# Kernel tuning notes

Measured on AMD Instinct MI355X. Metric: run time of the kernel, lower is better.

The kernel has to match this reference:

```python
import jax, jax.numpy as jnp
import numpy as np

N = 100000
E = 1600000
IN_DIM = 256
HID = 128
LAYERS = 8
ALPHA = 0.1
THETA = 0.5


def setup_inputs() -> dict:
    key = jax.random.key(0)
    ks = jax.random.split(key, 6)
    x = jax.random.normal(ks[0], (N, IN_DIM), dtype=jnp.float32)
    edge_index = jax.random.randint(ks[1], (2, E), 0, N, dtype=jnp.int64)
    W_in = jax.random.normal(ks[2], (IN_DIM, HID), dtype=jnp.float32) / np.sqrt(IN_DIM)
    b_in = jnp.zeros((HID,), dtype=jnp.float32)
    convs_W = jax.random.normal(ks[3], (LAYERS, HID, HID), dtype=jnp.float32) / np.sqrt(HID)
    W_out = jax.random.normal(ks[4], (HID, 1), dtype=jnp.float32) / np.sqrt(HID)
    b_out = jnp.zeros((1,), dtype=jnp.float32)
    return {"x": x, "edge_index": edge_index, "W_in": W_in, "b_in": b_in,
            "convs_W": convs_W, "W_out": W_out, "b_out": b_out}


def reference(x, edge_index, W_in, b_in, convs_W, W_out, b_out):
    row = edge_index[0]  # source nodes
    col = edge_index[1]  # destination nodes
    # gcn_norm with self-loops: deg = in-degree + 1
    deg = jax.ops.segment_sum(jnp.ones((E,), dtype=jnp.float32), col, num_segments=N) + 1.0
    dinv = jax.lax.rsqrt(deg)
    norm = dinv[row] * dinv[col]            # [E] edge weights
    self_norm = dinv * dinv                 # [N] self-loop weights (1/deg)

    def propagate(h):
        # Ahat @ h : gather-scale-scatter over edges + self-loop term
        msgs = h[row] * norm[:, None]       # [E, HID]
        return jax.ops.segment_sum(msgs, col, num_segments=N) + h * self_norm[:, None]

    h0 = jax.nn.relu(x @ W_in + b_in)       # initial residual
    h = h0
    for i in range(LAYERS):
        agg = propagate(h)
        s = (1.0 - ALPHA) * agg + ALPHA * h0
        beta = float(np.log(THETA / (i + 1) + 1.0))
        h = jax.nn.relu((1.0 - beta) * s + beta * (s @ convs_W[i]))
    return (h @ W_out + b_out).squeeze(-1)  # [N]
```

## Files before the change

### kernel.cpp

```cpp
#include <hip/hip_runtime.h>
#include <math.h>

#define HID 128
#define NB 32
#define SBST 136
#define CSH 9
#define MCH 8192
#define GOFF (32 * SBST)
#define CAP 1024

typedef unsigned int uint32;
typedef unsigned short ushort_t;
typedef __attribute__((ext_vector_type(8))) short bf16x8;
typedef __attribute__((ext_vector_type(4))) float f32x4;

__device__ __forceinline__ unsigned short f2bf(float f) {
    unsigned u = __float_as_uint(f);
    u += 0x7FFF + ((u >> 16) & 1);
    return (unsigned short)(u >> 16);
}
__device__ __forceinline__ float bf_lo(uint32 u) { return __uint_as_float(u << 16); }
__device__ __forceinline__ float bf_hi(uint32 u) { return __uint_as_float(u & 0xFFFF0000u); }

__global__ void degree_k(const int* __restrict__ col, int* __restrict__ counts, int E) {
    int e = blockIdx.x * 256 + threadIdx.x;
    if (e < E) atomicAdd(&counts[col[e]], 1);
}

__global__ void scan1_k(const int* __restrict__ counts, int* __restrict__ row_ptr,
                        int* __restrict__ blocksums, float* __restrict__ dinv, int N) {
    __shared__ int tmp[256];
    int t = threadIdx.x;
    int i = blockIdx.x * 256 + t;
    int v = (i < N) ? counts[i] : 0;
    if (i < N) dinv[i] = rsqrtf((float)v + 1.0f);
    tmp[t] = v;
    __syncthreads();
    for (int off = 1; off < 256; off <<= 1) {
        int x = (t >= off) ? tmp[t - off] : 0;
        __syncthreads();
        tmp[t] += x;
        __syncthreads();
    }
    if (i < N) row_ptr[i] = tmp[t] - v;
    if (t == 255) blocksums[blockIdx.x] = tmp[t];
}

__global__ void scan2_k(const int* __restrict__ blocksums, int* __restrict__ blockoffs, int nb) {
    __shared__ int tmp[512];
    int t = threadIdx.x;
    int v = (t < nb) ? blocksums[t] : 0;
    tmp[t] = v;
    __syncthreads();
    for (int off = 1; off < 512; off <<= 1) {
        int x = (t >= off) ? tmp[t - off] : 0;
        __syncthreads();
        tmp[t] += x;
        __syncthreads();
    }
    if (t < nb) blockoffs[t] = tmp[t] - v;
}

__global__ void scan3_k(int* __restrict__ row_ptr, int* __restrict__ cursor,
                        int* __restrict__ ccursor,
                        const int* __restrict__ blockoffs, int N, int E) {
    int i = blockIdx.x * 256 + threadIdx.x;
    if (i < N) {
        int v = row_ptr[i] + blockoffs[blockIdx.x];
        row_ptr[i] = v;
        cursor[i] = v;
        if ((i & ((1 << CSH) - 1)) == 0) ccursor[i >> CSH] = v;
    }
    if (i == 0) row_ptr[N] = E;
}

__global__ __launch_bounds__(256) void multisplit_k(const int* __restrict__ row,
                                                    const int* __restrict__ col,
                                                    int* __restrict__ ccursor,
                                                    int2* __restrict__ ebuf,
                                                    int E, int NCO) {
    __shared__ int lcnt[256];
    __shared__ int gbase[256];
    __shared__ int lpos[256];
    int t = threadIdx.x;
    int e0 = blockIdx.x * MCH;
    lcnt[t] = 0;
    lpos[t] = 0;
    __syncthreads();
    for (int i = t; i < MCH; i += 256) {
        int e = e0 + i;
        if (e < E) atomicAdd(&lcnt[col[e] >> CSH], 1);
    }
    __syncthreads();
    if (t < NCO && lcnt[t] > 0) gbase[t] = atomicAdd(&ccursor[t], lcnt[t]);
    __syncthreads();
    for (int i = t; i < MCH; i += 256) {
        int e = e0 + i;
        if (e < E) {
            int c = col[e];
            int b = c >> CSH;
            int p = atomicAdd(&lpos[b], 1);
            ebuf[gbase[b] + p] = make_int2(row[e], c);
        }
    }
}

__global__ void cfinal_k(const int2* __restrict__ ebuf, const int* __restrict__ row_ptr,
                         int* __restrict__ cursor, int* __restrict__ srcS, int N) {
    int b = blockIdx.x;
    int n0 = b << CSH;
    int n1 = n0 + (1 << CSH);
    if (n1 > N) n1 = N;
    int beg = row_ptr[n0];
    int end = row_ptr[n1];
    for (int i = beg + threadIdx.x; i < end; i += 256) {
        int2 p = ebuf[i];
        int pos = atomicAdd(&cursor[p.y], 1);
        srcS[pos] = p.x;
    }
}

__global__ void wprep_k(const float* __restrict__ convs, short* __restrict__ Wt) {
    int idx = blockIdx.x * 256 + threadIdx.x;
    if (idx >= 8 * 128 * 128) return;
    int l = idx >> 14;
    int r = idx & 16383;
    int k = r >> 7;
    int n = r & 127;
    float beta = logf(0.5f / (float)(l + 1) + 1.0f);
    float v = beta * convs[idx] + ((k == n) ? (1.0f - beta) : 0.0f);
    Wt[(l << 14) + (n << 7) + k] = (short)f2bf(v);
}

__global__ void winprep_k(const float* __restrict__ Win, short* __restrict__ Winb) {
    int idx = blockIdx.x * 256 + threadIdx.x;
    if (idx >= 256 * 128) return;
    int k = idx >> 7;
    int n = idx & 127;
    Winb[n * 256 + k] = (short)f2bf(Win[idx]);
}

__global__ __launch_bounds__(256) void h0_k(const float* __restrict__ x,
                                            const short* __restrict__ Winb,
                                            const float* __restrict__ bin,
                                            const float* __restrict__ dinv,
                                            ushort_t* __restrict__ h0b,
                                            ushort_t* __restrict__ g,
                                            int N) {
    __shared__ float xsf[NB * 256];
    __shared__ float s_dv[NB];
    int t = threadIdx.x;
    int lane = t & 63, wv = t >> 6;
    int base = blockIdx.x * NB;

    if (t < NB) s_dv[t] = (base + t < N) ? dinv[base + t] : 1.f;

    if (base + NB <= N) {
        const float* xblk = x + (size_t)base * 256;
#pragma unroll
        for (int it = 0; it < 8; it++) {
            int m = wv * 8 + it;
            const float* src = xblk + (size_t)m * 256 + ((lane ^ (m & 7)) << 2);
            __builtin_amdgcn_global_load_lds(
                (const __attribute__((address_space(1))) unsigned int*)src,
                (__attribute__((address_space(3))) unsigned int*)&xsf[m * 256],
                16, 0, 0);
        }
    } else {
        for (int idx = t; idx < NB * 64; idx += 256) {
            int m = idx >> 6;
            int c16 = idx & 63;
            int nn = base + m;
            float4 v = make_float4(0.f, 0.f, 0.f, 0.f);
            if (nn < N) v = *(const float4*)&x[(size_t)nn * 256 + c16 * 4];
            *(float4*)&xsf[m * 256 + ((c16 ^ (m & 7)) << 2)] = v;
        }
    }
    __syncthreads();

    int mt = (wv & 1) * 16;
    int jb = wv >> 1;
    int lrow = lane & 15;
    int lq = lane >> 4;
    int r = mt + lrow;
    f32x4 acc0 = {0.f, 0.f, 0.f, 0.f};
    f32x4 acc1 = {0.f, 0.f, 0.f, 0.f};
    f32x4 acc2 = {0.f, 0.f, 0.f, 0.f};
    f32x4 acc3 = {0.f, 0.f, 0.f, 0.f};
#pragma unroll
    for (int ks = 0; ks < 8; ks++) {
        int c16a = ks * 8 + lq * 2;
        f32x4 va = *(const f32x4*)&xsf[r * 256 + (((c16a + 0) ^ (r & 7)) << 2)];
        f32x4 vb = *(const f32x4*)&xsf[r * 256 + (((c16a + 1) ^ (r & 7)) << 2)];
        bf16x8 a;
        a[0] = (short)f2bf(va[0]); a[1] = (short)f2bf(va[1]);
        a[2] = (short)f2bf(va[2]); a[3] = (short)f2bf(va[3]);
        a[4] = (short)f2bf(vb[0]); a[5] = (short)f2bf(vb[1]);
        a[6] = (short)f2bf(vb[2]); a[7] = (short)f2bf(vb[3]);
        bf16x8 b0 = *(const bf16x8*)&Winb[((jb + 0) * 16 + lrow) * 256 + ks * 32 + lq * 8];
        bf16x8 b1 = *(const bf16x8*)&Winb[((jb + 2) * 16 + lrow) * 256 + ks * 32 + lq * 8];
        bf16x8 b2 = *(const bf16x8*)&Winb[((jb + 4) * 16 + lrow) * 256 + ks * 32 + lq * 8];
        bf16x8 b3 = *(const bf16x8*)&Winb[((jb + 6) * 16 + lrow) * 256 + ks * 32 + lq * 8];
        acc0 = __builtin_amdgcn_mfma_f32_16x16x32_bf16(a, b0, acc0, 0, 0, 0);
        acc1 = __builtin_amdgcn_mfma_f32_16x16x32_bf16(a, b1, acc1, 0, 0, 0);
        acc2 = __builtin_amdgcn_mfma_f32_16x16x32_bf16(a, b2, acc2, 0, 0, 0);
        acc3 = __builtin_amdgcn_mfma_f32_16x16x32_bf16(a, b3, acc3, 0, 0, 0);
    }

    __syncthreads();
    short* sb = (short*)xsf;
#pragma unroll
    for (int q = 0; q < 4; q++) {
        f32x4 accq = (q == 0) ? acc0 : (q == 1) ? acc1 : (q == 2) ? acc2 : acc3;
        int j0 = (jb + 2 * q) * 16;
        float bj = bin[j0 + lrow];
#pragma unroll
        for (int rr = 0; rr < 4; rr++) {
            int rowm = mt + lq * 4 + rr;
            float h = fmaxf(accq[rr] + bj, 0.f);
            sb[rowm * SBST + j0 + lrow] = (short)f2bf(h);
            sb[GOFF + rowm * SBST + j0 + lrow] = (short)f2bf(s_dv[rowm] * h);
        }
    }
    __syncthreads();
    for (int idx = t; idx < NB * 16; idx += 256) {
        int rowm = idx >> 4;
        int c = (idx & 15) * 8;
        int dst = base + rowm;
        if (dst < N) {
            *(bf16x8*)&h0b[(size_t)dst * HID + c] = *(const bf16x8*)&sb[rowm * SBST + c];
            *(bf16x8*)&g[(size_t)dst * HID + c]   = *(const bf16x8*)&sb[GOFF + rowm * SBST + c];
        }
    }
}

__global__ __launch_bounds__(256, 6) void layer_k(const ushort_t* __restrict__ g_in,
                                                  ushort_t* __restrict__ g_out,
                                                  const ushort_t* __restrict__ h0b,
                                                  const float* __restrict__ dinv,
                                                  const int* __restrict__ row_ptr,
                                                  const int* __restrict__ srcS,
                                                  const short* __restrict__ Wtb,
                                                  int N) {
    __shared__ int   s_idx[CAP + 16];
    __shared__ int   s_rp[NB + 1];
    __shared__ short s_bf[NB * SBST];
    __shared__ float s_dv[NB];
    int t = threadIdx.x;
    int lane = t & 63;
    int wv = t >> 6;
    int base = blockIdx.x * NB;

    if (t < NB + 1) s_rp[t] = row_ptr[min(base + t, N)];
    if (t < NB) s_dv[t] = (base + t < N) ? dinv[base + t] : 1.f;
    int blk_beg = row_ptr[base];
    int blk_end = row_ptr[min(base + NB, N)];
    int nE = blk_end - blk_beg;
    int nL = nE < CAP ? nE : CAP;
    for (int i = t; i < nL; i += 256) s_idx[i] = srcS[blk_beg + i];
    if (t < 16) s_idx[nL + t] = 0;
    __syncthreads();

    const char* gbp = (const char*)g_in;
    uint32 lb = (uint32)(lane << 2);
    for (int m = wv; m < NB; m += 4) {
        int dst = base + m;
        if (dst >= N) {
            *(uint32*)&s_bf[m * SBST + lane * 2] = 0;
            continue;
        }
        float dv = s_dv[m];
        uint32 gd = ((const uint32*)(g_in + (size_t)dst * HID))[lane];
        uint32 hu = ((const uint32*)(h0b + (size_t)dst * HID))[lane];
        float ax = bf_lo(gd), ay = bf_hi(gd);
        int beg = s_rp[m], end = s_rp[m + 1];
        int lend = end - blk_beg;
        if (lend <= CAP) {
            for (int e = beg - blk_beg; e < lend; e += 16) {
                int rem = lend - e;
                int i0  = s_idx[e + 0];
                int i1  = s_idx[e + 1];
                int i2  = s_idx[e + 2];
                int i3  = s_idx[e + 3];
                int i4  = s_idx[e + 4];
                int i5  = s_idx[e + 5];
                int i6  = s_idx[e + 6];
                int i7  = s_idx[e + 7];
                int i8  = s_idx[e + 8];
                int i9  = s_idx[e + 9];
                int i10 = s_idx[e + 10];
                int i11 = s_idx[e + 11];
                int i12 = s_idx[e + 12];
                int i13 = s_idx[e + 13];
                int i14 = s_idx[e + 14];
                int i15 = s_idx[e + 15];
                uint32 g0  = *(const uint32*)(gbp + (((uint32)i0  << 8) | lb));
                uint32 g1  = *(const uint32*)(gbp + (((uint32)i1  << 8) | lb));
                uint32 g2  = *(const uint32*)(gbp + (((uint32)i2  << 8) | lb));
                uint32 g3  = *(const uint32*)(gbp + (((uint32)i3  << 8) | lb));
                uint32 g4  = *(const uint32*)(gbp + (((uint32)i4  << 8) | lb));
                uint32 g5  = *(const uint32*)(gbp + (((uint32)i5  << 8) | lb));
                uint32 g6  = *(const uint32*)(gbp + (((uint32)i6  << 8) | lb));
                uint32 g7  = *(const uint32*)(gbp + (((uint32)i7  << 8) | lb));
                uint32 g8  = *(const uint32*)(gbp + (((uint32)i8  << 8) | lb));
                uint32 g9  = *(const uint32*)(gbp + (((uint32)i9  << 8) | lb));
                uint32 g10 = *(const uint32*)(gbp + (((uint32)i10 << 8) | lb));
                uint32 g11 = *(const uint32*)(gbp + (((uint32)i11 << 8) | lb));
                uint32 g12 = *(const uint32*)(gbp + (((uint32)i12 << 8) | lb));
                uint32 g13 = *(const uint32*)(gbp + (((uint32)i13 << 8) | lb));
                uint32 g14 = *(const uint32*)(gbp + (((uint32)i14 << 8) | lb));
                uint32 g15 = *(const uint32*)(gbp + (((uint32)i15 << 8) | lb));
                ax += bf_lo(g0); ay += bf_hi(g0);
                if (rem > 1)  { ax += bf_lo(g1);  ay += bf_hi(g1);  }
                if (rem > 2)  { ax += bf_lo(g2);  ay += bf_hi(g2);  }
                if (rem > 3)  { ax += bf_lo(g3);  ay += bf_hi(g3);  }
                if (rem > 4)  { ax += bf_lo(g4);  ay += bf_hi(g4);  }
                if (rem > 5)  { ax += bf_lo(g5);  ay += bf_hi(g5);  }
                if (rem > 6)  { ax += bf_lo(g6);  ay += bf_hi(g6);  }
                if (rem > 7)  { ax += bf_lo(g7);  ay += bf_hi(g7);  }
                if (rem > 8)  { ax += bf_lo(g8);  ay += bf_hi(g8);  }
                if (rem > 9)  { ax += bf_lo(g9);  ay += bf_hi(g9);  }
                if (rem > 10) { ax += bf_lo(g10); ay += bf_hi(g10); }
                if (rem > 11) { ax += bf_lo(g11); ay += bf_hi(g11); }
                if (rem > 12) { ax += bf_lo(g12); ay += bf_hi(g12); }
                if (rem > 13) { ax += bf_lo(g13); ay += bf_hi(g13); }
                if (rem > 14) { ax += bf_lo(g14); ay += bf_hi(g14); }
                if (rem > 15) { ax += bf_lo(g15); ay += bf_hi(g15); }
            }
        } else {
            for (int e = beg; e < end; e += 16) {
                int rem = end - e;
                int last = end - 1;
#pragma unroll
                for (int k = 0; k < 16; k++) {
                    if (k < rem) {
                        int ii = e + k;
                        int sn = srcS[ii > last ? last : ii];
                        uint32 gg = *(const uint32*)(gbp + (((uint32)sn << 8) | lb));
                        ax += bf_lo(gg); ay += bf_hi(gg);
                    }
                }
            }
        }
        float sc = 0.9f * dv;
        float sx = sc * ax + 0.1f * bf_lo(hu);
        float sy = sc * ay + 0.1f * bf_hi(hu);
        uint32 pk = ((uint32)f2bf(sy) << 16) | (uint32)f2bf(sx);
        *(uint32*)&s_bf[m * SBST + lane * 2] = pk;
    }
    __syncthreads();

    int mt = (wv & 1) * 16;
    int jb = wv >> 1;
    int lrow = lane & 15;
    int lq = lane >> 4;
    f32x4 acc0 = {0.f, 0.f, 0.f, 0.f};
    f32x4 acc1 = {0.f, 0.f, 0.f, 0.f};
    f32x4 acc2 = {0.f, 0.f, 0.f, 0.f};
    f32x4 acc3 = {0.f, 0.f, 0.f, 0.f};
#pragma unroll
    for (int ks = 0; ks < 4; ks++) {
        bf16x8 a = *(const bf16x8*)&s_bf[(mt + lrow) * SBST + ks * 32 + lq * 8];
        bf16x8 b0 = *(const bf16x8*)&Wtb[((jb + 0) * 16 + lrow) * 128 + ks * 32 + lq * 8];
        bf16x8 b1 = *(const bf16x8*)&Wtb[((jb + 2) * 16 + lrow) * 128 + ks * 32 + lq * 8];
        bf16x8 b2 = *(const bf16x8*)&Wtb[((jb + 4) * 16 + lrow) * 128 + ks * 32 + lq * 8];
        bf16x8 b3 = *(const bf16x8*)&Wtb[((jb + 6) * 16 + lrow) * 128 + ks * 32 + lq * 8];
        acc0 = __builtin_amdgcn_mfma_f32_16x16x32_bf16(a, b0, acc0, 0, 0, 0);
        acc1 = __builtin_amdgcn_mfma_f32_16x16x32_bf16(a, b1, acc1, 0, 0, 0);
        acc2 = __builtin_amdgcn_mfma_f32_16x16x32_bf16(a, b2, acc2, 0, 0, 0);
        acc3 = __builtin_amdgcn_mfma_f32_16x16x32_bf16(a, b3, acc3, 0, 0, 0);
    }

    __syncthreads();
#pragma unroll
    for (int q = 0; q < 4; q++) {
        f32x4 accq = (q == 0) ? acc0 : (q == 1) ? acc1 : (q == 2) ? acc2 : acc3;
        int j0 = (jb + 2 * q) * 16;
#pragma unroll
        for (int r = 0; r < 4; r++) {
            int rowm = mt + lq * 4 + r;
            float h = fmaxf(accq[r], 0.f);
            s_bf[rowm * SBST + j0 + lrow] = (short)f2bf(s_dv[rowm] * h);
        }
    }
    __syncthreads();
    for (int idx = t; idx < NB * 16; idx += 256) {
        int rowm = idx >> 4;
        int c = (idx & 15) * 8;
        int dst = base + rowm;
        if (dst < N)
            *(bf16x8*)&g_out[(size_t)dst * HID + c] = *(const bf16x8*)&s_bf[rowm * SBST + c];
    }
}

__global__ void out_k(const ushort_t* __restrict__ g, const float* __restrict__ dinv,
                      const float* __restrict__ Wout, const float* __restrict__ bout,
                      float* __restrict__ out, int N) {
    int t = threadIdx.x;
    int lane = t & 63;
    int wv = t >> 6;
    int n = blockIdx.x * 4 + wv;
    if (n >= N) return;
    uint32 u = ((const uint32*)(g + (size_t)n * HID))[lane];
    float v = bf_lo(u) * Wout[lane * 2] + bf_hi(u) * Wout[lane * 2 + 1];
#pragma unroll
    for (int off = 32; off > 0; off >>= 1) v += __shfl_down(v, off, 64);
    if (lane == 0) out[n] = v / dinv[n] + bout[0];
}

extern "C" void kernel_launch(void* const* d_in, const int* in_sizes, int n_in,
                              void* d_out, int out_size, void* d_ws, size_t ws_size,
                              hipStream_t stream) {
    const float* x    = (const float*)d_in[0];
    const int*   ei   = (const int*)d_in[1];
    const float* Win  = (const float*)d_in[2];
    const float* bin  = (const float*)d_in[3];
    const float* convs= (const float*)d_in[4];
    const float* Wout = (const float*)d_in[5];
    const float* bout = (const float*)d_in[6];

    int N = in_sizes[0] / 256;
    int E = in_sizes[1] / 2;
    const int* row = ei;
    const int* col = ei + E;

    char* ws = (char*)d_ws;
    size_t off = 0;
    auto alloc = [&](size_t bytes) -> char* {
        char* p = ws + off;
        off = (off + bytes + 255) & ~(size_t)255;
        return p;
    };
    int NCO = (N + (1 << CSH) - 1) >> CSH;
    int*      counts    = (int*)alloc((size_t)N * 4);
    int*      row_ptr   = (int*)alloc((size_t)(N + 1) * 4);
    int*      cursor    = (int*)alloc((size_t)N * 4);
    int*      ccursor   = (int*)alloc((size_t)NCO * 4);
    int*      blocksums = (int*)alloc(512 * 4);
    int*      blockoffs = (int*)alloc(512 * 4);
    float*    dinv      = (float*)alloc((size_t)N * 4);
    int*      srcS      = (int*)alloc((size_t)E * 4);
    short*    Wt        = (short*)alloc((size_t)8 * 128 * 128 * 2);
    short*    Winb      = (short*)alloc((size_t)256 * 128 * 2);
    ushort_t* h0b       = (ushort_t*)alloc((size_t)N * HID * 2);
    ushort_t* gA        = (ushort_t*)alloc((size_t)N * HID * 2);
    ushort_t* gB        = (ushort_t*)alloc((size_t)N * HID * 2);
    int2*     ebuf      = (int2*)gB;

    int eb = (E + 255) / 256;
    int nb = (N + 255) / 256;
    int mb = (E + MCH - 1) / MCH;

    hipMemsetAsync(counts, 0, (size_t)N * 4, stream);
    degree_k<<<eb, 256, 0, stream>>>(col, counts, E);
    scan1_k<<<nb, 256, 0, stream>>>(counts, row_ptr, blocksums, dinv, N);
    scan2_k<<<1, 512, 0, stream>>>(blocksums, blockoffs, nb);
    scan3_k<<<nb, 256, 0, stream>>>(row_ptr, cursor, ccursor, blockoffs, N, E);
    multisplit_k<<<mb, 256, 0, stream>>>(row, col, ccursor, ebuf, E, NCO);
    cfinal_k<<<NCO, 256, 0, stream>>>(ebuf, row_ptr, cursor, srcS, N);
    wprep_k<<<512, 256, 0, stream>>>(convs, Wt);
    winprep_k<<<128, 256, 0, stream>>>(Win, Winb);

    int gb = (N + NB - 1) / NB;
    h0_k<<<gb, 256, 0, stream>>>(x, Winb, bin, dinv, h0b, gA, N);

    ushort_t* gin = gA;
    ushort_t* gout = gB;
    for (int i = 0; i < 8; i++) {
        layer_k<<<gb, 256, 0, stream>>>(gin, gout, h0b, dinv, row_ptr, srcS,
                                        Wt + (size_t)i * 128 * 128, N);
        ushort_t* tp = gin; gin = gout; gout = tp;
    }
    out_k<<<(N + 3) / 4, 256, 0, stream>>>(gin, dinv, Wout, bout, (float*)d_out, N);
}
```

Before: 1.006 ms.

## Gather two edges per wave with 8-byte lanes and half-wave reduction

The aggregation loop now splits each wave into two halves. Each half gathers a different edge's 256-byte row using 8-byte loads per lane, and the halves are combined with a cross-half shuffle. Partial tail groups are padded by repeating the last neighbor, and the surplus copies are subtracted afterward, so the per-edge branches go away. Launch bounds are lowered to 4 waves per SIMD to allow more registers for the wider gathers, which may reduce occupancy. The correction also adds rounding differences from subtracting repeated bf16 values.

```diff
diff --git a/kernel.cpp b/kernel.cpp
--- a/kernel.cpp
+++ b/kernel.cpp
@@ -234,7 +234,7 @@
     }
 }
 
-__global__ __launch_bounds__(256, 6) void layer_k(const ushort_t* __restrict__ g_in,
+__global__ __launch_bounds__(256, 4) void layer_k(const ushort_t* __restrict__ g_in,
                                                   ushort_t* __restrict__ g_out,
                                                   const ushort_t* __restrict__ h0b,
                                                   const float* __restrict__ dinv,
@@ -242,7 +242,7 @@
                                                   const int* __restrict__ srcS,
                                                   const short* __restrict__ Wtb,
                                                   int N) {
-    __shared__ int   s_idx[CAP + 16];
+    __shared__ int   s_idx[CAP];
     __shared__ int   s_rp[NB + 1];
     __shared__ short s_bf[NB * SBST];
     __shared__ float s_dv[NB];
@@ -258,95 +258,126 @@
     int nE = blk_end - blk_beg;
     int nL = nE < CAP ? nE : CAP;
     for (int i = t; i < nL; i += 256) s_idx[i] = srcS[blk_beg + i];
-    if (t < 16) s_idx[nL + t] = 0;
     __syncthreads();
 
     const char* gbp = (const char*)g_in;
-    uint32 lb = (uint32)(lane << 2);
+    const char* hbp = (const char*)h0b;
+    int c = lane & 31;
+    int half = lane >> 5;
+    uint32 cb = (uint32)(c << 3);
+
     for (int m = wv; m < NB; m += 4) {
         int dst = base + m;
         if (dst >= N) {
-            *(uint32*)&s_bf[m * SBST + lane * 2] = 0;
+            if (lane < 32) *(uint2*)&s_bf[m * SBST + c * 4] = make_uint2(0u, 0u);
             continue;
         }
         float dv = s_dv[m];
-        uint32 gd = ((const uint32*)(g_in + (size_t)dst * HID))[lane];
-        uint32 hu = ((const uint32*)(h0b + (size_t)dst * HID))[lane];
-        float ax = bf_lo(gd), ay = bf_hi(gd);
+        uint2 sg = make_uint2(0u, 0u), sh = make_uint2(0u, 0u);
+        if (lane < 32) {
+            sg = *(const uint2*)(gbp + (((size_t)dst) << 8) + cb);
+            sh = *(const uint2*)(hbp + (((size_t)dst) << 8) + cb);
+        }
         int beg = s_rp[m], end = s_rp[m + 1];
-        int lend = end - blk_beg;
-        if (lend <= CAP) {
-            for (int e = beg - blk_beg; e < lend; e += 16) {
-                int rem = lend - e;
-                int i0  = s_idx[e + 0];
-                int i1  = s_idx[e + 1];
-                int i2  = s_idx[e + 2];
-                int i3  = s_idx[e + 3];
-                int i4  = s_idx[e + 4];
-                int i5  = s_idx[e + 5];
-                int i6  = s_idx[e + 6];
-                int i7  = s_idx[e + 7];
-                int i8  = s_idx[e + 8];
-                int i9  = s_idx[e + 9];
-                int i10 = s_idx[e + 10];
-                int i11 = s_idx[e + 11];
-                int i12 = s_idx[e + 12];
-                int i13 = s_idx[e + 13];
-                int i14 = s_idx[e + 14];
-                int i15 = s_idx[e + 15];
-                uint32 g0  = *(const uint32*)(gbp + (((uint32)i0  << 8) | lb));
-                uint32 g1  = *(const uint32*)(gbp + (((uint32)i1  << 8) | lb));
-                uint32 g2  = *(const uint32*)(gbp + (((uint32)i2  << 8) | lb));
-                uint32 g3  = *(const uint32*)(gbp + (((uint32)i3  << 8) | lb));
-                uint32 g4  = *(const uint32*)(gbp + (((uint32)i4  << 8) | lb));
-                uint32 g5  = *(const uint32*)(gbp + (((uint32)i5  << 8) | lb));
-                uint32 g6  = *(const uint32*)(gbp + (((uint32)i6  << 8) | lb));
-                uint32 g7  = *(const uint32*)(gbp + (((uint32)i7  << 8) | lb));
-                uint32 g8  = *(const uint32*)(gbp + (((uint32)i8  << 8) | lb));
-                uint32 g9  = *(const uint32*)(gbp + (((uint32)i9  << 8) | lb));
-                uint32 g10 = *(const uint32*)(gbp + (((uint32)i10 << 8) | lb));
-                uint32 g11 = *(const uint32*)(gbp + (((uint32)i11 << 8) | lb));
-                uint32 g12 = *(const uint32*)(gbp + (((uint32)i12 << 8) | lb));
-                uint32 g13 = *(const uint32*)(gbp + (((uint32)i13 << 8) | lb));
-                uint32 g14 = *(const uint32*)(gbp + (((uint32)i14 << 8) | lb));
-                uint32 g15 = *(const uint32*)(gbp + (((uint32)i15 << 8) | lb));
-                ax += bf_lo(g0); ay += bf_hi(g0);
-                if (rem > 1)  { ax += bf_lo(g1);  ay += bf_hi(g1);  }
-                if (rem > 2)  { ax += bf_lo(g2);  ay += bf_hi(g2);  }
-                if (rem > 3)  { ax += bf_lo(g3);  ay += bf_hi(g3);  }
-                if (rem > 4)  { ax += bf_lo(g4);  ay += bf_hi(g4);  }
-                if (rem > 5)  { ax += bf_lo(g5);  ay += bf_hi(g5);  }
-                if (rem > 6)  { ax += bf_lo(g6);  ay += bf_hi(g6);  }
-                if (rem > 7)  { ax += bf_lo(g7);  ay += bf_hi(g7);  }
-                if (rem > 8)  { ax += bf_lo(g8);  ay += bf_hi(g8);  }
-                if (rem > 9)  { ax += bf_lo(g9);  ay += bf_hi(g9);  }
-                if (rem > 10) { ax += bf_lo(g10); ay += bf_hi(g10); }
-                if (rem > 11) { ax += bf_lo(g11); ay += bf_hi(g11); }
-                if (rem > 12) { ax += bf_lo(g12); ay += bf_hi(g12); }
-                if (rem > 13) { ax += bf_lo(g13); ay += bf_hi(g13); }
-                if (rem > 14) { ax += bf_lo(g14); ay += bf_hi(g14); }
-                if (rem > 15) { ax += bf_lo(g15); ay += bf_hi(g15); }
-            }
-        } else {
-            for (int e = beg; e < end; e += 16) {
-                int rem = end - e;
-                int last = end - 1;
-#pragma unroll
-                for (int k = 0; k < 16; k++) {
-                    if (k < rem) {
-                        int ii = e + k;
-                        int sn = srcS[ii > last ? last : ii];
-                        uint32 gg = *(const uint32*)(gbp + (((uint32)sn << 8) | lb));
-                        ax += bf_lo(gg); ay += bf_hi(gg);
+        int deg = end - beg;
+        float a0 = 0.f, a1 = 0.f, a2 = 0.f, a3 = 0.f;
+        bool fastp = (end - blk_beg) <= nL;
+        if (deg > 0) {
+            int nfull = deg >> 4;
+            if (fastp) {
+                int e = beg - blk_beg;
+                int lastI = e + deg - 1;
+                for (int r = 0; r < nfull; ++r, e += 16) {
+                    int ixx[8];
+#pragma unroll
+                    for (int p = 0; p < 8; p++) ixx[p] = s_idx[e + 2 * p + half];
+                    uint2 gvv[8];
+#pragma unroll
+                    for (int p = 0; p < 8; p++)
+                        gvv[p] = *(const uint2*)(gbp + (((size_t)(uint32)ixx[p]) << 8) + cb);
+#pragma unroll
+                    for (int p = 0; p < 8; p++) {
+                        a0 += bf_lo(gvv[p].x); a1 += bf_hi(gvv[p].x);
+                        a2 += bf_lo(gvv[p].y); a3 += bf_hi(gvv[p].y);
+                    }
+                }
+                if (deg & 15) {
+                    int ixx[8];
+#pragma unroll
+                    for (int p = 0; p < 8; p++) {
+                        int sl = e + 2 * p + half;
+                        ixx[p] = s_idx[sl < lastI ? sl : lastI];
+                    }
+                    uint2 gvv[8];
+#pragma unroll
+                    for (int p = 0; p < 8; p++)
+                        gvv[p] = *(const uint2*)(gbp + (((size_t)(uint32)ixx[p]) << 8) + cb);
+#pragma unroll
+                    for (int p = 0; p < 8; p++) {
+                        a0 += bf_lo(gvv[p].x); a1 += bf_hi(gvv[p].x);
+                        a2 += bf_lo(gvv[p].y); a3 += bf_hi(gvv[p].y);
+                    }
+                }
+            } else {
+                int e = beg;
+                int lastA = end - 1;
+                for (int r = 0; r < nfull; ++r, e += 16) {
+                    int ixx[8];
+#pragma unroll
+                    for (int p = 0; p < 8; p++) ixx[p] = srcS[e + 2 * p + half];
+                    uint2 gvv[8];
+#pragma unroll
+                    for (int p = 0; p < 8; p++)
+                        gvv[p] = *(const uint2*)(gbp + (((size_t)(uint32)ixx[p]) << 8) + cb);
+#pragma unroll
+                    for (int p = 0; p < 8; p++) {
+                        a0 += bf_lo(gvv[p].x); a1 += bf_hi(gvv[p].x);
+                        a2 += bf_lo(gvv[p].y); a3 += bf_hi(gvv[p].y);
+                    }
+                }
+                if (deg & 15) {
+                    int ixx[8];
+#pragma unroll
+                    for (int p = 0; p < 8; p++) {
+                        int sl = e + 2 * p + half;
+                        ixx[p] = srcS[sl < lastA ? sl : lastA];
+                    }
+                    uint2 gvv[8];
+#pragma unroll
+                    for (int p = 0; p < 8; p++)
+                        gvv[p] = *(const uint2*)(gbp + (((size_t)(uint32)ixx[p]) << 8) + cb);
+#pragma unroll
+                    for (int p = 0; p < 8; p++) {
+                        a0 += bf_lo(gvv[p].x); a1 += bf_hi(gvv[p].x);
+                        a2 += bf_lo(gvv[p].y); a3 += bf_hi(gvv[p].y);
                     }
                 }
             }
-        }
-        float sc = 0.9f * dv;
-        float sx = sc * ax + 0.1f * bf_lo(hu);
-        float sy = sc * ay + 0.1f * bf_hi(hu);
-        uint32 pk = ((uint32)f2bf(sy) << 16) | (uint32)f2bf(sx);
-        *(uint32*)&s_bf[m * SBST + lane * 2] = pk;
+            a0 += __shfl_xor(a0, 32, 64);
+            a1 += __shfl_xor(a1, 32, 64);
+            a2 += __shfl_xor(a2, 32, 64);
+            a3 += __shfl_xor(a3, 32, 64);
+            if (deg & 15) {
+                int cnt = ((nfull + 1) << 4) - deg;
+                int ixL = fastp ? s_idx[beg - blk_beg + deg - 1] : srcS[end - 1];
+                uint2 gl = make_uint2(0u, 0u);
+                if (lane < 32) gl = *(const uint2*)(gbp + (((size_t)(uint32)ixL) << 8) + cb);
+                float fc = (float)cnt;
+                a0 -= fc * bf_lo(gl.x); a1 -= fc * bf_hi(gl.x);
+                a2 -= fc * bf_lo(gl.y); a3 -= fc * bf_hi(gl.y);
+            }
+        }
+        if (lane < 32) {
+            float sc = 0.9f * dv;
+            float s0 = sc * (a0 + bf_lo(sg.x)) + 0.1f * bf_lo(sh.x);
+            float s1 = sc * (a1 + bf_hi(sg.x)) + 0.1f * bf_hi(sh.x);
+            float s2 = sc * (a2 + bf_lo(sg.y)) + 0.1f * bf_lo(sh.y);
+            float s3 = sc * (a3 + bf_hi(sg.y)) + 0.1f * bf_hi(sh.y);
+            uint2 pk;
+            pk.x = ((uint32)f2bf(s1) << 16) | (uint32)f2bf(s0);
+            pk.y = ((uint32)f2bf(s3) << 16) | (uint32)f2bf(s2);
+            *(uint2*)&s_bf[m * SBST + c * 4] = pk;
+        }
     }
     __syncthreads();
 
@@ -386,10 +417,10 @@
     __syncthreads();
     for (int idx = t; idx < NB * 16; idx += 256) {
         int rowm = idx >> 4;
-        int c = (idx & 15) * 8;
+        int cc = (idx & 15) * 8;
         int dst = base + rowm;
         if (dst < N)
-            *(bf16x8*)&g_out[(size_t)dst * HID + c] = *(const bf16x8*)&s_bf[rowm * SBST + c];
+            *(bf16x8*)&g_out[(size_t)dst * HID + cc] = *(const bf16x8*)&s_bf[rowm * SBST + cc];
     }
 }
 
```

Result: no change. 1.020 ms (+1.4%).

## Gather neighbor rows via global_load_lds into per-wave LDS slabs

Applied to the files above, without the earlier changes.

Replaces the register-based 16-way unrolled neighbor gather with direct global-to-LDS loads (global_load_lds) into a per-wave 16-row slab, then sums the rows from LDS. Padded slots are clamped to the last edge and over-counted contributions are subtracted afterwards, which removes the per-element rem branches. The intent is to cut VGPR pressure and issue overhead in the gather. In exchange it adds 16 KB of LDS, drops the launch-bounds occupancy hint from 6 to 4, and forces a full vmcnt(0) wait per batch of 16, which can reduce memory-level parallelism. The subtraction correction also adds bf16 rounding differences.

```diff
diff --git a/kernel.cpp b/kernel.cpp
--- a/kernel.cpp
+++ b/kernel.cpp
@@ -234,7 +234,7 @@
     }
 }
 
-__global__ __launch_bounds__(256, 6) void layer_k(const ushort_t* __restrict__ g_in,
+__global__ __launch_bounds__(256, 4) void layer_k(const ushort_t* __restrict__ g_in,
                                                   ushort_t* __restrict__ g_out,
                                                   const ushort_t* __restrict__ h0b,
                                                   const float* __restrict__ dinv,
@@ -242,7 +242,8 @@
                                                   const int* __restrict__ srcS,
                                                   const short* __restrict__ Wtb,
                                                   int N) {
-    __shared__ int   s_idx[CAP + 16];
+    __shared__ short slab[4][16 * 128];
+    __shared__ int   s_idx[CAP];
     __shared__ int   s_rp[NB + 1];
     __shared__ short s_bf[NB * SBST];
     __shared__ float s_dv[NB];
@@ -258,11 +259,12 @@
     int nE = blk_end - blk_beg;
     int nL = nE < CAP ? nE : CAP;
     for (int i = t; i < nL; i += 256) s_idx[i] = srcS[blk_beg + i];
-    if (t < 16) s_idx[nL + t] = 0;
     __syncthreads();
 
     const char* gbp = (const char*)g_in;
-    uint32 lb = (uint32)(lane << 2);
+    const char* lanebase = gbp + (lane << 2);
+    short* myslab = &slab[wv][0];
+
     for (int m = wv; m < NB; m += 4) {
         int dst = base + m;
         if (dst >= N) {
@@ -272,79 +274,47 @@
         float dv = s_dv[m];
         uint32 gd = ((const uint32*)(g_in + (size_t)dst * HID))[lane];
         uint32 hu = ((const uint32*)(h0b + (size_t)dst * HID))[lane];
-        float ax = bf_lo(gd), ay = bf_hi(gd);
+        float a0 = bf_lo(gd), a1 = bf_hi(gd);
         int beg = s_rp[m], end = s_rp[m + 1];
-        int lend = end - blk_beg;
-        if (lend <= CAP) {
-            for (int e = beg - blk_beg; e < lend; e += 16) {
-                int rem = lend - e;
-                int i0  = s_idx[e + 0];
-                int i1  = s_idx[e + 1];
-                int i2  = s_idx[e + 2];
-                int i3  = s_idx[e + 3];
-                int i4  = s_idx[e + 4];
-                int i5  = s_idx[e + 5];
-                int i6  = s_idx[e + 6];
-                int i7  = s_idx[e + 7];
-                int i8  = s_idx[e + 8];
-                int i9  = s_idx[e + 9];
-                int i10 = s_idx[e + 10];
-                int i11 = s_idx[e + 11];
-                int i12 = s_idx[e + 12];
-                int i13 = s_idx[e + 13];
-                int i14 = s_idx[e + 14];
-                int i15 = s_idx[e + 15];
-                uint32 g0  = *(const uint32*)(gbp + (((uint32)i0  << 8) | lb));
-                uint32 g1  = *(const uint32*)(gbp + (((uint32)i1  << 8) | lb));
-                uint32 g2  = *(const uint32*)(gbp + (((uint32)i2  << 8) | lb));
-                uint32 g3  = *(const uint32*)(gbp + (((uint32)i3  << 8) | lb));
-                uint32 g4  = *(const uint32*)(gbp + (((uint32)i4  << 8) | lb));
-                uint32 g5  = *(const uint32*)(gbp + (((uint32)i5  << 8) | lb));
-                uint32 g6  = *(const uint32*)(gbp + (((uint32)i6  << 8) | lb));
-                uint32 g7  = *(const uint32*)(gbp + (((uint32)i7  << 8) | lb));
-                uint32 g8  = *(const uint32*)(gbp + (((uint32)i8  << 8) | lb));
-                uint32 g9  = *(const uint32*)(gbp + (((uint32)i9  << 8) | lb));
-                uint32 g10 = *(const uint32*)(gbp + (((uint32)i10 << 8) | lb));
-                uint32 g11 = *(const uint32*)(gbp + (((uint32)i11 << 8) | lb));
-                uint32 g12 = *(const uint32*)(gbp + (((uint32)i12 << 8) | lb));
-                uint32 g13 = *(const uint32*)(gbp + (((uint32)i13 << 8) | lb));
-                uint32 g14 = *(const uint32*)(gbp + (((uint32)i14 << 8) | lb));
-                uint32 g15 = *(const uint32*)(gbp + (((uint32)i15 << 8) | lb));
-                ax += bf_lo(g0); ay += bf_hi(g0);
-                if (rem > 1)  { ax += bf_lo(g1);  ay += bf_hi(g1);  }
-                if (rem > 2)  { ax += bf_lo(g2);  ay += bf_hi(g2);  }
-                if (rem > 3)  { ax += bf_lo(g3);  ay += bf_hi(g3);  }
-                if (rem > 4)  { ax += bf_lo(g4);  ay += bf_hi(g4);  }
-                if (rem > 5)  { ax += bf_lo(g5);  ay += bf_hi(g5);  }
-                if (rem > 6)  { ax += bf_lo(g6);  ay += bf_hi(g6);  }
-                if (rem > 7)  { ax += bf_lo(g7);  ay += bf_hi(g7);  }
-                if (rem > 8)  { ax += bf_lo(g8);  ay += bf_hi(g8);  }
-                if (rem > 9)  { ax += bf_lo(g9);  ay += bf_hi(g9);  }
-                if (rem > 10) { ax += bf_lo(g10); ay += bf_hi(g10); }
-                if (rem > 11) { ax += bf_lo(g11); ay += bf_hi(g11); }
-                if (rem > 12) { ax += bf_lo(g12); ay += bf_hi(g12); }
-                if (rem > 13) { ax += bf_lo(g13); ay += bf_hi(g13); }
-                if (rem > 14) { ax += bf_lo(g14); ay += bf_hi(g14); }
-                if (rem > 15) { ax += bf_lo(g15); ay += bf_hi(g15); }
+        int deg = end - beg;
+        bool fastp = (end - blk_beg) <= nL;
+        if (deg > 0) {
+            int nR = (deg + 15) >> 4;
+            int eb0 = beg - blk_beg;
+            int lastSlot = deg - 1;
+            for (int r = 0; r < nR; r++) {
+                int s0 = r << 4;
+#pragma unroll
+                for (int j = 0; j < 16; j++) {
+                    int sl = s0 + j;
+                    if (sl > lastSlot) sl = lastSlot;
+                    int idx = fastp ? s_idx[eb0 + sl] : srcS[beg + sl];
+                    const char* src = lanebase + ((size_t)(uint32)idx << 8);
+                    __builtin_amdgcn_global_load_lds(
+                        (const __attribute__((address_space(1))) unsigned int*)src,
+                        (__attribute__((address_space(3))) unsigned int*)&myslab[j * 128],
+                        4, 0, 0);
+                }
+                asm volatile("s_waitcnt vmcnt(0)" ::: "memory");
+                __builtin_amdgcn_sched_barrier(0);
+#pragma unroll
+                for (int j = 0; j < 16; j++) {
+                    uint32 v = *(const uint32*)&myslab[j * 128 + lane * 2];
+                    a0 += bf_lo(v); a1 += bf_hi(v);
+                }
+                __builtin_amdgcn_sched_barrier(0);
             }
-        } else {
-            for (int e = beg; e < end; e += 16) {
-                int rem = end - e;
-                int last = end - 1;
-#pragma unroll
-                for (int k = 0; k < 16; k++) {
-                    if (k < rem) {
-                        int ii = e + k;
-                        int sn = srcS[ii > last ? last : ii];
-                        uint32 gg = *(const uint32*)(gbp + (((uint32)sn << 8) | lb));
-                        ax += bf_lo(gg); ay += bf_hi(gg);
-                    }
-                }
+            int cnt = (nR << 4) - deg;
+            if (cnt > 0) {
+                uint32 v = *(const uint32*)&myslab[(lastSlot & 15) * 128 + lane * 2];
+                float fc = (float)cnt;
+                a0 -= fc * bf_lo(v);
+                a1 -= fc * bf_hi(v);
             }
         }
         float sc = 0.9f * dv;
-        float sx = sc * ax + 0.1f * bf_lo(hu);
-        float sy = sc * ay + 0.1f * bf_hi(hu);
+        float sx = sc * a0 + 0.1f * bf_lo(hu);
+        float sy = sc * a1 + 0.1f * bf_hi(hu);
         uint32 pk = ((uint32)f2bf(sy) << 16) | (uint32)f2bf(sx);
         *(uint32*)&s_bf[m * SBST + lane * 2] = pk;
     }
@@ -386,10 +356,10 @@
     __syncthreads();
     for (int idx = t; idx < NB * 16; idx += 256) {
         int rowm = idx >> 4;
-        int c = (idx & 15) * 8;
+        int cc = (idx & 15) * 8;
         int dst = base + rowm;
         if (dst < N)
-            *(bf16x8*)&g_out[(size_t)dst * HID + c] = *(const bf16x8*)&s_bf[rowm * SBST + c];
+            *(bf16x8*)&g_out[(size_t)dst * HID + cc] = *(const bf16x8*)&s_bf[rowm * SBST + cc];
     }
 }
 
```

Result: slower. 2.158 ms (+114.4%).
